# Kernel tuning notes

Measured on AMD Instinct MI355X. Metric: run time of the kernel, lower is better.

The kernel has to match this reference:

```python
import jax, jax.numpy as jnp
import numpy as np

B, SQ, SKV = 32, 200, 200
D, HEADS, L, V, FF = 1024, 16, 6, 32000, 2048
HD = D // HEADS
EPS = 1e-9


def _pe(seq_len, d):
    # sinusoidal positional encoding, matching PositionalEncoding
    pos = jnp.arange(seq_len, dtype=jnp.float32)[:, None]
    div = jnp.power(10000.0, jnp.arange(0, d, 2, dtype=jnp.float32) / d)
    ang = pos / div
    pe = jnp.zeros((seq_len, d), dtype=jnp.float32)
    pe = pe.at[:, 0::2].set(jnp.sin(ang))
    pe = pe.at[:, 1::2].set(jnp.cos(ang))
    return pe


def _ln(x, g, b):
    m = x.mean(-1, keepdims=True)
    v = ((x - m) ** 2).mean(-1, keepdims=True)  # unbiased=False
    return (x - m) / jnp.sqrt(v + EPS) * g + b


def _mha(xq, xk, xv, Wq, bq, Wk, bk, Wv, bv, Wo, mask):
    b, sq, _ = xq.shape
    sk = xk.shape[1]
    q = (xq @ Wq + bq).reshape(b, sq, HEADS, HD).transpose(0, 2, 1, 3)
    k = (xk @ Wk + bk).reshape(b, sk, HEADS, HD).transpose(0, 2, 1, 3)
    v = (xv @ Wv + bv).reshape(b, sk, HEADS, HD).transpose(0, 2, 1, 3)
    scores = jnp.einsum('bhqd,bhkd->bhqk', q, k) / jnp.float32(np.sqrt(HD))
    if mask is not None:
        scores = jnp.where(mask, -jnp.inf, scores)
    attn = jax.nn.softmax(scores, axis=-1)
    o = jnp.einsum('bhqk,bhkd->bhqd', attn, v).transpose(0, 2, 1, 3).reshape(b, sq, D)
    return o @ Wo


def setup_inputs() -> dict:
    key0 = jax.random.key(0)
    ks = list(jax.random.split(key0, 24))
    s = 0.02
    inp = {}
    # token ids in [1, V): avoid pad id 0 so no fully-masked softmax row (NaN)
    inp['query'] = jax.random.randint(ks[0], (B, SQ), 1, V)
    inp['key'] = jax.random.normal(ks[1], (B, SKV, D), jnp.float32)
    inp['value'] = jax.random.normal(ks[2], (B, SKV, D), jnp.float32)
    inp['emb'] = jax.random.normal(ks[3], (V, D), jnp.float32) * s
    for i, nm in enumerate(['ln1_g', 'ln2_g', 'ln3_g']):
        inp[nm] = jnp.ones((L, D), jnp.float32)
    for nm in ['ln1_b', 'ln2_b', 'ln3_b']:
        inp[nm] = jnp.zeros((L, D), jnp.float32)
    names = ['Wq_s', 'Wk_s', 'Wv_s', 'Wo_s', 'Wq_c', 'Wk_c', 'Wv_c', 'Wo_c']
    for i, nm in enumerate(names):
        inp[nm] = jax.random.normal(ks[4 + i], (L, D, D), jnp.float32) * s
    for nm in ['bq_s', 'bk_s', 'bv_s', 'bq_c', 'bk_c', 'bv_c']:
        inp[nm] = jnp.zeros((L, D), jnp.float32)
    inp['W1'] = jax.random.normal(ks[12], (L, D, FF), jnp.float32) * s
    inp['bf1'] = jnp.zeros((L, FF), jnp.float32)
    inp['W2'] = jax.random.normal(ks[13], (L, FF, D), jnp.float32) * s
    inp['bf2'] = jnp.zeros((L, D), jnp.float32)
    inp['lnf_g'] = jnp.ones((D,), jnp.float32)
    inp['lnf_b'] = jnp.zeros((D,), jnp.float32)
    return inp


def reference(query, key, value, emb, ln1_g, ln1_b, ln2_g, ln2_b, ln3_g, ln3_b,
              Wq_s, bq_s, Wk_s, bk_s, Wv_s, bv_s, Wo_s,
              Wq_c, bq_c, Wk_c, bk_c, Wv_c, bv_c, Wo_c,
              W1, bf1, W2, bf2, lnf_g, lnf_b):
    x = emb[query] + _pe(SQ, D)[None]  # dropout is identity at eval
    causal = jnp.triu(jnp.ones((SQ, SQ), dtype=bool), 1)[None, None]
    pad = (query == 0)[:, None, None, :]
    self_mask = causal | pad  # [B,1,SQ,SQ]
    o = x
    for l in range(L):
        qn = _ln(o, ln1_g[l], ln1_b[l])
        sa = _mha(qn, qn, qn, Wq_s[l], bq_s[l], Wk_s[l], bk_s[l], Wv_s[l], bv_s[l], Wo_s[l], self_mask)
        o1 = o + sa
        an = _ln(o1, ln2_g[l], ln2_b[l])
        ca = _mha(an, key, value, Wq_c[l], bq_c[l], Wk_c[l], bk_c[l], Wv_c[l], bv_c[l], Wo_c[l], None)
        o2 = o1 + ca
        cn = _ln(o2, ln3_g[l], ln3_b[l])
        ff = jax.nn.relu(cn @ W1[l] + bf1[l]) @ W2[l] + bf2[l]
        o = o2 + ff
    return _ln(o, lnf_g, lnf_b)
```

## Files before the change

kernel.cpp:

```cpp
#include <hip/hip_runtime.h>
#include <math.h>

#define BB  32
#define SQl 200
#define SKV 200
#define DD  1024
#define NH  16
#define HDm 64
#define NL  6
#define FFD 2048

typedef __attribute__((ext_vector_type(8))) short  short8v;
typedef __attribute__((ext_vector_type(4))) float  floatx4;

__device__ __forceinline__ ushort f2bf(float x) {
  uint u = __builtin_bit_cast(uint, x);
  u = (u + 0x7FFFu + ((u >> 16) & 1u)) >> 16;
  return (ushort)u;
}

__device__ __forceinline__ void gll16(const void* g, void* l) {
  __builtin_amdgcn_global_load_lds((const __attribute__((address_space(1))) void*)g,
                                   (__attribute__((address_space(3))) void*)l,
                                   16, 0, 0);
}

__global__ __launch_bounds__(256) void embed_pe_kernel(const int* __restrict__ qids,
                                                       const float* __restrict__ emb,
                                                       float* __restrict__ x) {
  int idx = blockIdx.x * 256 + threadIdx.x;
  int d   = idx & (DD - 1);
  int row = idx >> 10;
  int s   = row % SQl;
  int tok = qids[row];
  float expo = (float)(d & ~1) * (1.0f / (float)DD);
  float dv   = powf(10000.0f, expo);
  float ang  = (float)s / dv;
  float pe   = (d & 1) ? cosf(ang) : sinf(ang);
  x[idx] = emb[(size_t)tok * DD + d] + pe;
}

__global__ __launch_bounds__(256) void cvt_bf16_kernel(const float* __restrict__ in,
                                                       ushort* __restrict__ out, int n8) {
  int idx = blockIdx.x * 256 + threadIdx.x;
  if (idx >= n8) return;
  const floatx4 va = ((const floatx4*)in)[idx * 2];
  const floatx4 vb = ((const floatx4*)in)[idx * 2 + 1];
  short8v o;
  o[0] = (short)f2bf(va.x); o[1] = (short)f2bf(va.y);
  o[2] = (short)f2bf(va.z); o[3] = (short)f2bf(va.w);
  o[4] = (short)f2bf(vb.x); o[5] = (short)f2bf(vb.y);
  o[6] = (short)f2bf(vb.z); o[7] = (short)f2bf(vb.w);
  ((short8v*)out)[idx] = o;
}

struct P8 { const float* p[8]; };
__global__ __launch_bounds__(256) void transpose48_kernel(P8 srcs, ushort* __restrict__ dst) {
  __shared__ float t[32][33];
  const size_t MEL = (size_t)DD * DD;
  const int z = blockIdx.z;
  const int arr = z / 6, l = z - arr * 6;
  const size_t base[8] = {0, MEL, 2*MEL, 18*MEL, 24*MEL, 30*MEL, 36*MEL, 42*MEL};
  const size_t lstr[8] = {3*MEL, 3*MEL, 3*MEL, MEL, MEL, MEL, MEL, MEL};
  const float* __restrict__ W = srcs.p[arr] + (size_t)l * MEL;
  ushort* __restrict__ WT = dst + base[arr] + (size_t)l * lstr[arr];
  const int n0 = blockIdx.x * 32, k0 = blockIdx.y * 32;
  const int tx = threadIdx.x & 31, ty = threadIdx.x >> 5;
#pragma unroll
  for (int i = 0; i < 4; ++i)
    t[ty + i * 8][tx] = W[(size_t)(k0 + ty + i * 8) * DD + n0 + tx];
  __syncthreads();
#pragma unroll
  for (int i = 0; i < 4; ++i)
    WT[(size_t)(n0 + ty + i * 8) * DD + k0 + tx] = f2bf(t[tx][ty + i * 8]);
}

__global__ __launch_bounds__(256) void transposeW_kernel(const float* __restrict__ src,
                                                         ushort* __restrict__ dst,
                                                         int K, int N) {
  __shared__ float t[32][33];
  const int z = blockIdx.z;
  const float* __restrict__ W = src + (size_t)z * K * N;
  ushort* __restrict__ WT = dst + (size_t)z * K * N;
  const int n0 = blockIdx.x * 32, k0 = blockIdx.y * 32;
  const int tx = threadIdx.x & 31, ty = threadIdx.x >> 5;
#pragma unroll
  for (int i = 0; i < 4; ++i)
    t[ty + i * 8][tx] = W[(size_t)(k0 + ty + i * 8) * N + n0 + tx];
  __syncthreads();
#pragma unroll
  for (int i = 0; i < 4; ++i)
    WT[(size_t)(n0 + ty + i * 8) * K + k0 + tx] = f2bf(t[tx][ty + i * 8]);
}

template <int OBF16>
__global__ __launch_bounds__(256) void ln4_kernel(const float* __restrict__ in,
                                                  const float* __restrict__ gam,
                                                  const float* __restrict__ bet,
                                                  float* __restrict__ outf,
                                                  ushort* __restrict__ outb) {
  const int wid  = threadIdx.x >> 6;
  const int lane = threadIdx.x & 63;
  const int row  = blockIdx.x * 4 + wid;
  const float* ip = in + (size_t)row * DD;

  float4 x[4];
  float s = 0.f, sq = 0.f;
#pragma unroll
  for (int i = 0; i < 4; ++i) {
    x[i] = *(const float4*)&ip[i * 256 + lane * 4];
    s  += x[i].x + x[i].y + x[i].z + x[i].w;
    sq += x[i].x * x[i].x + x[i].y * x[i].y + x[i].z * x[i].z + x[i].w * x[i].w;
  }
#pragma unroll
  for (int msk = 1; msk < 64; msk <<= 1) {
    s  += __shfl_xor(s,  msk, 64);
    sq += __shfl_xor(sq, msk, 64);
  }
  const float m   = s * (1.0f / (float)DD);
  const float var = sq * (1.0f / (float)DD) - m * m;
  const float inv = rsqrtf(var + 1e-9f);

#pragma unroll
  for (int i = 0; i < 4; ++i) {
    const int c = i * 256 + lane * 4;
    const float4 g4 = *(const float4*)&gam[c];
    const float4 b4 = *(const float4*)&bet[c];
    float o0 = (x[i].x - m) * inv * g4.x + b4.x;
    float o1 = (x[i].y - m) * inv * g4.y + b4.y;
    float o2 = (x[i].z - m) * inv * g4.z + b4.z;
    float o3 = (x[i].w - m) * inv * g4.w + b4.w;
    if (OBF16) {
      uint2 pk;
      pk.x = (uint)f2bf(o0) | ((uint)f2bf(o1) << 16);
      pk.y = (uint)f2bf(o2) | ((uint)f2bf(o3) << 16);
      *(uint2*)&outb[(size_t)row * DD + c] = pk;
    } else {
      float4 ov; ov.x = o0; ov.y = o1; ov.z = o2; ov.w = o3;
      *(float4*)&outf[(size_t)row * DD + c] = ov;
    }
  }
}

struct BiasP { const float* p[6]; };
template <int RELU, int ACC, int OBF16>
__global__ __launch_bounds__(256) void gemm_mfma(const ushort* __restrict__ A,
                                                 const ushort* __restrict__ BT,
                                                 BiasP bias,
                                                 float* __restrict__ C,
                                                 ushort* __restrict__ Cb,
                                                 int M, int N, int K, int ldc) {
  __shared__ short8v As[1024];
  __shared__ short8v Bs[1024];
  const int tid  = threadIdx.x;
  const int wid  = tid >> 6;
  const int lane = tid & 63;
  const int bm = blockIdx.y * 128;
  const int bn = blockIdx.x * 128;
  const int wm = (wid >> 1) * 64;
  const int wn = (wid & 1) * 64;
  const int lq = lane & 15;
  const int lg = lane >> 4;

  const int base0 = wid * 64;
  const ushort* aS[4];
  const ushort* bS[4];
#pragma unroll
  for (int i = 0; i < 4; ++i) {
    const int s   = base0 + 256 * i + lane;
    const int row = s >> 3;
    const int kg  = (s & 7) ^ (row & 7);
    aS[i] = A  + (size_t)(bm + row) * K + kg * 8;
    bS[i] = BT + (size_t)(bn + row) * K + kg * 8;
  }

  int aIdx[4], bIdx[4];
#pragma unroll
  for (int i = 0; i < 4; ++i) {
    const int mr = wm + i * 16 + lq;
    aIdx[i] = mr * 8 + (lg ^ (mr & 7));
    const int nr = wn + i * 16 + lq;
    bIdx[i] = nr * 8 + (lg ^ (nr & 7));
  }

  floatx4 acc[4][4];
  const floatx4 fz = {0.f, 0.f, 0.f, 0.f};
#pragma unroll
  for (int mi = 0; mi < 4; ++mi)
#pragma unroll
    for (int ni = 0; ni < 4; ++ni) acc[mi][ni] = fz;

  for (int k0 = 0; k0 < K; k0 += 64) {
#pragma unroll
    for (int i = 0; i < 4; ++i) gll16(aS[i] + k0, &As[base0 + 256 * i]);
#pragma unroll
    for (int i = 0; i < 4; ++i) gll16(bS[i] + k0, &Bs[base0 + 256 * i]);
    __syncthreads();
#pragma unroll
    for (int kk = 0; kk < 2; ++kk) {
      short8v af[4], bf_[4];
#pragma unroll
      for (int i = 0; i < 4; ++i) {
        af[i]  = As[aIdx[i] ^ (kk * 4)];
        bf_[i] = Bs[bIdx[i] ^ (kk * 4)];
      }
#pragma unroll
      for (int mi = 0; mi < 4; ++mi)
#pragma unroll
        for (int ni = 0; ni < 4; ++ni)
          acc[mi][ni] = __builtin_amdgcn_mfma_f32_16x16x32_bf16(af[mi], bf_[ni], acc[mi][ni], 0, 0, 0);
    }
    __syncthreads();
  }

#pragma unroll
  for (int mi = 0; mi < 4; ++mi) {
    const int row = bm + wm + mi * 16 + lg * 4;
#pragma unroll
    for (int ni = 0; ni < 4; ++ni) {
      const int col = bn + wn + ni * 16 + lq;
      const float* bp = bias.p[col >> 10];
      const float bvv = bp ? bp[col & (DD - 1)] : 0.f;
#pragma unroll
      for (int r = 0; r < 4; ++r) {
        float val = acc[mi][ni][r] + bvv;
        if (ACC)  val += C[(size_t)(row + r) * ldc + col];
        if (RELU) val = fmaxf(val, 0.f);
        if (OBF16) Cb[(size_t)(row + r) * ldc + col] = f2bf(val);
        else       C [(size_t)(row + r) * ldc + col] = val;
      }
    }
  }
}

static inline void launch_g(const ushort* A, const ushort* BT, BiasP bias,
                            float* C, ushort* Cb, int M, int N, int K, int ldc,
                            int mode, hipStream_t s) {
  dim3 grid(N / 128, M / 128), blk(256);
  if (mode == 1)      gemm_mfma<0, 1, 0><<<grid, blk, 0, s>>>(A, BT, bias, C, Cb, M, N, K, ldc);
  else if (mode == 2) gemm_mfma<1, 0, 1><<<grid, blk, 0, s>>>(A, BT, bias, C, Cb, M, N, K, ldc);
  else                gemm_mfma<0, 0, 1><<<grid, blk, 0, s>>>(A, BT, bias, C, Cb, M, N, K, ldc);
}

template <int CAUSAL>
__global__ __launch_bounds__(256, 2) void attn_mfma_kernel(const ushort* __restrict__ q, int qs,
                                                           const ushort* __restrict__ k, int ks,
                                                           const ushort* __restrict__ v, int vs,
                                                           const int* __restrict__ qids,
                                                           ushort* __restrict__ out) {
  __shared__ short8v Kl[208 * 8];
  __shared__ ushort  Vt[64 * 256];
  __shared__ short8v Pl[1024];
  __shared__ float   padf[224];

  const int bh   = blockIdx.x;
  const int h    = bh & (NH - 1);
  const int b    = bh >> 4;
  const int tid  = threadIdx.x;
  const int w    = tid >> 6;
  const int lane = tid & 63;
  const int lq   = lane & 15;
  const int lg   = lane >> 4;

  if (tid < 208) {
    const int kp = tid;
    if (kp < SKV) {
      const short8v* src = (const short8v*)(k + ((size_t)(b * SKV + kp)) * ks + h * HDm);
#pragma unroll
      for (int s = 0; s < 8; ++s) Kl[kp * 8 + (s ^ (kp & 7))] = src[s];
    } else {
      const short8v z = {0, 0, 0, 0, 0, 0, 0, 0};
#pragma unroll
      for (int s = 0; s < 8; ++s) Kl[kp * 8 + s] = z;
    }
  }
  if (tid < 224) {
    const int kp = tid;
    float pf = 1.f;
    if (kp < SKV) {
      pf = CAUSAL ? ((qids[b * SQl + kp] == 0) ? 1.f : 0.f) : 0.f;
      const short8v* src = (const short8v*)(v + ((size_t)(b * SKV + kp)) * vs + h * HDm);
      const int s3 = kp >> 3, k7 = kp & 7;
#pragma unroll
      for (int li = 0; li < 8; ++li) {
        const short8v vv = src[li];
#pragma unroll
        for (int e = 0; e < 8; ++e)
          Vt[(li * 8 + e) * 256 + ((s3 ^ e) * 8) + k7] = (ushort)vv[e];
      }
    } else {
      const int s3 = kp >> 3, k7 = kp & 7;
#pragma unroll
      for (int li = 0; li < 8; ++li)
#pragma unroll
        for (int e = 0; e < 8; ++e)
          Vt[(li * 8 + e) * 256 + ((s3 ^ e) * 8) + k7] = 0;
    }
    padf[kp] = pf;
  }
  __syncthreads();

  short8v qf[4][2];
#pragma unroll
  for (int i = 0; i < 4; ++i) {
    const int mt = i * 4 + w;
    if (mt > 12) continue;
    int qrow = mt * 16 + lq;
    if (qrow > SQl - 1) qrow = SQl - 1;
    const ushort* qp = q + ((size_t)(b * SQl + qrow)) * qs + h * HDm + lg * 8;
    qf[i][0] = *(const short8v*)qp;
    qf[i][1] = *(const short8v*)(qp + 32);
  }

  float rmax[4][4];
#pragma unroll
  for (int i = 0; i < 4; ++i)
#pragma unroll
    for (int r = 0; r < 4; ++r) rmax[i][r] = -3e38f;

  for (int kt = 0; kt < 13; ++kt) {
    const int kp = kt * 16 + lq;
    const short8v bk0 = Kl[kp * 8 + (lg ^ (kp & 7))];
    const short8v bk1 = Kl[kp * 8 + ((4 + lg) ^ (kp & 7))];
    const float pmask = padf[kp];
#pragma unroll
    for (int i = 0; i < 4; ++i) {
      const int mt = i * 4 + w;
      if (mt > 12) continue;
      floatx4 S = {0.f, 0.f, 0.f, 0.f};
      S = __builtin_amdgcn_mfma_f32_16x16x32_bf16(qf[i][0], bk0, S, 0, 0, 0);
      S = __builtin_amdgcn_mfma_f32_16x16x32_bf16(qf[i][1], bk1, S, 0, 0, 0);
#pragma unroll
      for (int r = 0; r < 4; ++r) {
        const int qrow = mt * 16 + lg * 4 + r;
        bool masked = (pmask != 0.f);
        if (CAUSAL) masked = masked || (kp > qrow);
        const float s = masked ? -3e38f : S[r] * 0.125f;
        rmax[i][r] = fmaxf(rmax[i][r], s);
      }
    }
  }
#pragma unroll
  for (int msk = 1; msk < 16; msk <<= 1)
#pragma unroll
    for (int i = 0; i < 4; ++i)
#pragma unroll
      for (int r = 0; r < 4; ++r)
        rmax[i][r] = fmaxf(rmax[i][r], __shfl_xor(rmax[i][r], msk, 64));

  float rsum[4][4];
  floatx4 Of[4][4];
  const floatx4 fz = {0.f, 0.f, 0.f, 0.f};
#pragma unroll
  for (int i = 0; i < 4; ++i)
#pragma unroll
    for (int r = 0; r < 4; ++r) { rsum[i][r] = 0.f; Of[i][r] = fz; }

  for (int kc = 0; kc < 7; ++kc) {
#pragma unroll
    for (int t = 0; t < 2; ++t) {
      const int kt = kc * 2 + t;
      const int kp = kt * 16 + lq;
      short8v bk0, bk1;
      float pmask = 1.f;
      if (kt < 13) {
        bk0 = Kl[kp * 8 + (lg ^ (kp & 7))];
        bk1 = Kl[kp * 8 + ((4 + lg) ^ (kp & 7))];
        pmask = padf[kp];
      }
#pragma unroll
      for (int i = 0; i < 4; ++i) {
        const int mt = i * 4 + w;
        if (mt > 12) continue;
        floatx4 S = {0.f, 0.f, 0.f, 0.f};
        if (kt < 13) {
          S = __builtin_amdgcn_mfma_f32_16x16x32_bf16(qf[i][0], bk0, S, 0, 0, 0);
          S = __builtin_amdgcn_mfma_f32_16x16x32_bf16(qf[i][1], bk1, S, 0, 0, 0);
        }
#pragma unroll
        for (int r = 0; r < 4; ++r) {
          const int qrow = mt * 16 + lg * 4 + r;
          bool masked = (kt >= 13) || (pmask != 0.f);
          if (CAUSAL) masked = masked || (kp > qrow);
          const float p = masked ? 0.f : __expf(S[r] * 0.125f - rmax[i][r]);
          rsum[i][r] += p;
          const int qrl  = lg * 4 + r;
          const int kpl  = t * 16 + lq;
          const int slot = (kpl >> 3) ^ ((qrl >> 2) & 3);
          ((ushort*)Pl)[(w * 4 + i) * 512 + qrl * 32 + slot * 8 + (kpl & 7)] = f2bf(p);
        }
      }
    }
    short8v vb[4];
#pragma unroll
    for (int dt = 0; dt < 4; ++dt) {
      const int d  = dt * 16 + lq;
      const int sk = kc * 4 + lg;
      vb[dt] = ((const short8v*)Vt)[d * 32 + (sk ^ (d & 7))];
    }
#pragma unroll
    for (int i = 0; i < 4; ++i) {
      const int mt = i * 4 + w;
      if (mt > 12) continue;
      const short8v pa = Pl[(w * 4 + i) * 64 + lq * 4 + (lg ^ ((lq >> 2) & 3))];
#pragma unroll
      for (int dt = 0; dt < 4; ++dt)
        Of[i][dt] = __builtin_amdgcn_mfma_f32_16x16x32_bf16(pa, vb[dt], Of[i][dt], 0, 0, 0);
    }
  }

#pragma unroll
  for (int msk = 1; msk < 16; msk <<= 1)
#pragma unroll
    for (int i = 0; i < 4; ++i)
#pragma unroll
      for (int r = 0; r < 4; ++r)
        rsum[i][r] += __shfl_xor(rsum[i][r], msk, 64);

#pragma unroll
  for (int i = 0; i < 4; ++i) {
    const int mt = i * 4 + w;
    if (mt > 12) continue;
#pragma unroll
    for (int r = 0; r < 4; ++r) {
      const int qrow = mt * 16 + lg * 4 + r;
      if (qrow >= SQl) continue;
      const float linv = 1.0f / rsum[i][r];
      ushort* op = out + ((size_t)(b * SQl + qrow)) * DD + h * HDm;
#pragma unroll
      for (int dt = 0; dt < 4; ++dt)
        op[dt * 16 + lq] = f2bf(Of[i][dt][r] * linv);
    }
  }
}

extern "C" void kernel_launch(void* const* d_in, const int* in_sizes, int n_in,
                              void* d_out, int out_size, void* d_ws, size_t ws_size,
                              hipStream_t stream) {
  (void)in_sizes; (void)n_in; (void)out_size; (void)ws_size;

  const int*   qids  = (const int*)  d_in[0];
  const float* key   = (const float*)d_in[1];
  const float* value = (const float*)d_in[2];
  const float* emb   = (const float*)d_in[3];
  const float* ln1_g = (const float*)d_in[4];
  const float* ln2_g = (const float*)d_in[5];
  const float* ln3_g = (const float*)d_in[6];
  const float* ln1_b = (const float*)d_in[7];
  const float* ln2_b = (const float*)d_in[8];
  const float* ln3_b = (const float*)d_in[9];
  const float* Wq_s  = (const float*)d_in[10];
  const float* Wk_s  = (const float*)d_in[11];
  const float* Wv_s  = (const float*)d_in[12];
  const float* Wo_s  = (const float*)d_in[13];
  const float* Wq_c  = (const float*)d_in[14];
  const float* Wk_c  = (const float*)d_in[15];
  const float* Wv_c  = (const float*)d_in[16];
  const float* Wo_c  = (const float*)d_in[17];
  const float* bq_s  = (const float*)d_in[18];
  const float* bk_s  = (const float*)d_in[19];
  const float* bv_s  = (const float*)d_in[20];
  const float* bq_c  = (const float*)d_in[21];
  const float* bk_c  = (const float*)d_in[22];
  const float* bv_c  = (const float*)d_in[23];
  const float* W1    = (const float*)d_in[24];
  const float* bf1   = (const float*)d_in[25];
  const float* W2    = (const float*)d_in[26];
  const float* bf2   = (const float*)d_in[27];
  const float* lnf_g = (const float*)d_in[28];
  const float* lnf_b = (const float*)d_in[29];

  const size_t NTOK = (size_t)BB * SQl * DD;
  const size_t MEL  = (size_t)DD * DD;
  char* w = (char*)d_ws;
  float*  o    = (float*)w;  w += NTOK * 4;
  ushort* t0b  = (ushort*)w; w += NTOK * 2;
  ushort* qkv  = (ushort*)w; w += (size_t)BB * SQl * 3 * DD * 2;
  ushort* kc   = (ushort*)w; w += (size_t)BB * SQl * 6 * DD * 2;
  ushort* vc   = (ushort*)w; w += (size_t)BB * SQl * 6 * DD * 2;
  ushort* kb   = (ushort*)w; w += NTOK * 2;
  ushort* vb   = (ushort*)w; w += NTOK * 2;
  ushort* fbb  = (ushort*)w; w += (size_t)BB * SQl * FFD * 2;
  ushort* wt   = (ushort*)w; w += 48 * MEL * 2;
  ushort* wt1  = (ushort*)w; w += (size_t)NL * DD * FFD * 2;
  ushort* wt2  = (ushort*)w; w += (size_t)NL * FFD * DD * 2;

  const int M = BB * SQl;
  const BiasP nob = {{nullptr, nullptr, nullptr, nullptr, nullptr, nullptr}};

  embed_pe_kernel<<<(int)(NTOK / 256), 256, 0, stream>>>(qids, emb, o);
  cvt_bf16_kernel<<<(int)(NTOK / 8 + 255) / 256, 256, 0, stream>>>(key,   kb, (int)(NTOK / 8));
  cvt_bf16_kernel<<<(int)(NTOK / 8 + 255) / 256, 256, 0, stream>>>(value, vb, (int)(NTOK / 8));

  P8 p8 = {{Wq_s, Wk_s, Wv_s, Wo_s, Wq_c, Wk_c, Wv_c, Wo_c}};
  transpose48_kernel<<<dim3(32, 32, 48), 256, 0, stream>>>(p8, wt);
  transposeW_kernel<<<dim3(FFD / 32, DD / 32, NL), 256, 0, stream>>>(W1, wt1, DD, FFD);
  transposeW_kernel<<<dim3(DD / 32, FFD / 32, NL), 256, 0, stream>>>(W2, wt2, FFD, DD);

  ushort* wtQKV = wt;
  ushort* wtOs  = wt + 18 * MEL;
  ushort* wtQc  = wt + 24 * MEL;
  ushort* wtKc  = wt + 30 * MEL;
  ushort* wtVc  = wt + 36 * MEL;
  ushort* wtOc  = wt + 42 * MEL;

  {
    BiasP bk6, bv6;
#pragma unroll
    for (int l = 0; l < NL; ++l) { bk6.p[l] = bk_c + l * DD; bv6.p[l] = bv_c + l * DD; }
    launch_g(kb, wtKc, bk6, nullptr, kc, M, 6 * DD, DD, 6 * DD, 3, stream);
    launch_g(vb, wtVc, bv6, nullptr, vc, M, 6 * DD, DD, 6 * DD, 3, stream);
  }

  for (int l = 0; l < NL; ++l) {
    ln4_kernel<1><<<M / 4, 256, 0, stream>>>(o, ln1_g + l * DD, ln1_b + l * DD, nullptr, t0b);
    BiasP bqkv = {{bq_s + l * DD, bk_s + l * DD, bv_s + l * DD, nullptr, nullptr, nullptr}};
    launch_g(t0b, wtQKV + l * 3 * MEL, bqkv, nullptr, qkv, M, 3 * DD, DD, 3 * DD, 3, stream);
    attn_mfma_kernel<1><<<BB * NH, 256, 0, stream>>>(qkv, 3 * DD, qkv + DD, 3 * DD,
                                                     qkv + 2 * DD, 3 * DD, qids, t0b);
    launch_g(t0b, wtOs + l * MEL, nob, o, nullptr, M, DD, DD, DD, 1, stream);

    ln4_kernel<1><<<M / 4, 256, 0, stream>>>(o, ln2_g + l * DD, ln2_b + l * DD, nullptr, t0b);
    BiasP bqc = {{bq_c + l * DD, nullptr, nullptr, nullptr, nullptr, nullptr}};
    launch_g(t0b, wtQc + l * MEL, bqc, nullptr, qkv, M, DD, DD, 3 * DD, 3, stream);
    attn_mfma_kernel<0><<<BB * NH, 256, 0, stream>>>(qkv, 3 * DD, kc + l * DD, 6 * DD,
                                                     vc + l * DD, 6 * DD, nullptr, t0b);
    launch_g(t0b, wtOc + l * MEL, nob, o, nullptr, M, DD, DD, DD, 1, stream);

    ln4_kernel<1><<<M / 4, 256, 0, stream>>>(o, ln3_g + l * DD, ln3_b + l * DD, nullptr, t0b);
    BiasP bf1p = {{bf1 + l * FFD, bf1 + l * FFD + DD, nullptr, nullptr, nullptr, nullptr}};
    launch_g(t0b, wt1 + (size_t)l * DD * FFD, bf1p, nullptr, fbb, M, FFD, DD, FFD, 2, stream);
    BiasP bf2p = {{bf2 + l * DD, nullptr, nullptr, nullptr, nullptr, nullptr}};
    launch_g(fbb, wt2 + (size_t)l * FFD * DD, bf2p, o, nullptr, M, DD, FFD, DD, 1, stream);
  }

  ln4_kernel<0><<<M / 4, 256, 0, stream>>>(o, lnf_g, lnf_b, (float*)d_out, nullptr);
}
```

Before: 2.711 ms.

## Rewrite GEMM as 8-wave 256x128 tile with triple-buffered async LDS pipeline

```diff
diff --git a/kernel.cpp b/kernel.cpp
--- a/kernel.cpp
+++ b/kernel.cpp
@@ -12,6 +12,10 @@
 
 typedef __attribute__((ext_vector_type(8))) short  short8v;
 typedef __attribute__((ext_vector_type(4))) float  floatx4;
+
+#define SBAR()  asm volatile("s_barrier" ::: "memory")
+#define VMCNT6() asm volatile("s_waitcnt vmcnt(6)" ::: "memory")
+#define VMCNT0() asm volatile("s_waitcnt vmcnt(0)" ::: "memory")
 
 __device__ __forceinline__ ushort f2bf(float x) {
   uint u = __builtin_bit_cast(uint, x);
@@ -144,33 +148,38 @@
 
 struct BiasP { const float* p[6]; };
 template <int RELU, int ACC, int OBF16>
-__global__ __launch_bounds__(256) void gemm_mfma(const ushort* __restrict__ A,
-                                                 const ushort* __restrict__ BT,
-                                                 BiasP bias,
-                                                 float* __restrict__ C,
-                                                 ushort* __restrict__ Cb,
-                                                 int M, int N, int K, int ldc) {
-  __shared__ short8v As[1024];
-  __shared__ short8v Bs[1024];
+__global__ __launch_bounds__(512) void gemm8_mfma(const ushort* __restrict__ A,
+                                                  const ushort* __restrict__ BT,
+                                                  BiasP bias,
+                                                  float* __restrict__ C,
+                                                  ushort* __restrict__ Cb,
+                                                  int M, int N, int K, int ldc) {
+  __shared__ short8v As[3 * 2048];
+  __shared__ short8v Bs[3 * 1024];
   const int tid  = threadIdx.x;
-  const int wid  = tid >> 6;
+  const int w    = tid >> 6;
   const int lane = tid & 63;
-  const int bm = blockIdx.y * 128;
+  const int bm = blockIdx.y * 256;
   const int bn = blockIdx.x * 128;
-  const int wm = (wid >> 1) * 64;
-  const int wn = (wid & 1) * 64;
+  const int wm = (w >> 1) * 64;
+  const int wn = (w & 1) * 64;
   const int lq = lane & 15;
   const int lg = lane >> 4;
 
-  const int base0 = wid * 64;
   const ushort* aS[4];
-  const ushort* bS[4];
+  const ushort* bS[2];
 #pragma unroll
   for (int i = 0; i < 4; ++i) {
-    const int s   = base0 + 256 * i + lane;
+    const int s   = w * 64 + i * 512 + lane;
     const int row = s >> 3;
     const int kg  = (s & 7) ^ (row & 7);
-    aS[i] = A  + (size_t)(bm + row) * K + kg * 8;
+    aS[i] = A + (size_t)(bm + row) * K + kg * 8;
+  }
+#pragma unroll
+  for (int i = 0; i < 2; ++i) {
+    const int s   = w * 64 + i * 512 + lane;
+    const int row = s >> 3;
+    const int kg  = (s & 7) ^ (row & 7);
     bS[i] = BT + (size_t)(bn + row) * K + kg * 8;
   }
 
@@ -190,27 +199,67 @@
 #pragma unroll
     for (int ni = 0; ni < 4; ++ni) acc[mi][ni] = fz;
 
-  for (int k0 = 0; k0 < K; k0 += 64) {
-#pragma unroll
-    for (int i = 0; i < 4; ++i) gll16(aS[i] + k0, &As[base0 + 256 * i]);
-#pragma unroll
-    for (int i = 0; i < 4; ++i) gll16(bS[i] + k0, &Bs[base0 + 256 * i]);
-    __syncthreads();
-#pragma unroll
-    for (int kk = 0; kk < 2; ++kk) {
-      short8v af[4], bf_[4];
-#pragma unroll
-      for (int i = 0; i < 4; ++i) {
-        af[i]  = As[aIdx[i] ^ (kk * 4)];
-        bf_[i] = Bs[bIdx[i] ^ (kk * 4)];
-      }
-#pragma unroll
-      for (int mi = 0; mi < 4; ++mi)
-#pragma unroll
-        for (int ni = 0; ni < 4; ++ni)
-          acc[mi][ni] = __builtin_amdgcn_mfma_f32_16x16x32_bf16(af[mi], bf_[ni], acc[mi][ni], 0, 0, 0);
-    }
-    __syncthreads();
+  const int nt = K >> 6;
+
+#pragma unroll
+  for (int b = 0; b < 2; ++b) {
+    const int koff = b * 64;
+    gll16(aS[0] + koff, &As[b * 2048 + w * 64 + 0 * 512]);
+    gll16(aS[1] + koff, &As[b * 2048 + w * 64 + 1 * 512]);
+    gll16(aS[2] + koff, &As[b * 2048 + w * 64 + 2 * 512]);
+    gll16(aS[3] + koff, &As[b * 2048 + w * 64 + 3 * 512]);
+    gll16(bS[0] + koff, &Bs[b * 1024 + w * 64 + 0 * 512]);
+    gll16(bS[1] + koff, &Bs[b * 1024 + w * 64 + 1 * 512]);
+  }
+  VMCNT6();
+  SBAR();
+
+  int cur = 0;
+  for (int t = 0; t < nt; ++t) {
+    int b2 = cur + 2; if (b2 >= 3) b2 -= 3;
+    const int koff2 = (t + 2) * 64;
+    const bool pf = (t + 2) < nt;
+    const int cbA = cur * 2048, cbB = cur * 1024;
+    short8v* dA = &As[b2 * 2048 + w * 64];
+    short8v* dB = &Bs[b2 * 1024 + w * 64];
+
+    short8v af[4], bf_[4];
+#pragma unroll
+    for (int i = 0; i < 4; ++i) { af[i] = As[cbA + aIdx[i]]; bf_[i] = Bs[cbB + bIdx[i]]; }
+    if (pf) {
+      gll16(aS[0] + koff2, dA + 0 * 512);
+      gll16(aS[1] + koff2, dA + 1 * 512);
+      gll16(bS[0] + koff2, dB + 0 * 512);
+    }
+    SBAR();
+    __builtin_amdgcn_s_setprio(1);
+#pragma unroll
+    for (int mi = 0; mi < 4; ++mi)
+#pragma unroll
+      for (int ni = 0; ni < 4; ++ni)
+        acc[mi][ni] = __builtin_amdgcn_mfma_f32_16x16x32_bf16(af[mi], bf_[ni], acc[mi][ni], 0, 0, 0);
+    __builtin_amdgcn_s_setprio(0);
+    SBAR();
+
+#pragma unroll
+    for (int i = 0; i < 4; ++i) { af[i] = As[cbA + (aIdx[i] ^ 4)]; bf_[i] = Bs[cbB + (bIdx[i] ^ 4)]; }
+    if (pf) {
+      gll16(aS[2] + koff2, dA + 2 * 512);
+      gll16(aS[3] + koff2, dA + 3 * 512);
+      gll16(bS[1] + koff2, dB + 1 * 512);
+    }
+    SBAR();
+    __builtin_amdgcn_s_setprio(1);
+#pragma unroll
+    for (int mi = 0; mi < 4; ++mi)
+#pragma unroll
+      for (int ni = 0; ni < 4; ++ni)
+        acc[mi][ni] = __builtin_amdgcn_mfma_f32_16x16x32_bf16(af[mi], bf_[ni], acc[mi][ni], 0, 0, 0);
+    __builtin_amdgcn_s_setprio(0);
+
+    if (pf) { VMCNT6(); } else { VMCNT0(); }
+    SBAR();
+    cur = cur + 1; if (cur >= 3) cur -= 3;
   }
 
 #pragma unroll
@@ -236,10 +285,10 @@
 static inline void launch_g(const ushort* A, const ushort* BT, BiasP bias,
                             float* C, ushort* Cb, int M, int N, int K, int ldc,
                             int mode, hipStream_t s) {
-  dim3 grid(N / 128, M / 128), blk(256);
-  if (mode == 1)      gemm_mfma<0, 1, 0><<<grid, blk, 0, s>>>(A, BT, bias, C, Cb, M, N, K, ldc);
-  else if (mode == 2) gemm_mfma<1, 0, 1><<<grid, blk, 0, s>>>(A, BT, bias, C, Cb, M, N, K, ldc);
-  else                gemm_mfma<0, 0, 1><<<grid, blk, 0, s>>>(A, BT, bias, C, Cb, M, N, K, ldc);
+  dim3 grid(N / 128, M / 256), blk(512);
+  if (mode == 1)      gemm8_mfma<0, 1, 0><<<grid, blk, 0, s>>>(A, BT, bias, C, Cb, M, N, K, ldc);
+  else if (mode == 2) gemm8_mfma<1, 0, 1><<<grid, blk, 0, s>>>(A, BT, bias, C, Cb, M, N, K, ldc);
+  else                gemm8_mfma<0, 0, 1><<<grid, blk, 0, s>>>(A, BT, bias, C, Cb, M, N, K, ldc);
 }
 
 template <int CAUSAL>
```

Result: faster. 2.633 ms (-2.9%).
